# Kernel optimization log

Measured on AMD Instinct MI355X. Metric: run time of the kernel, lower is better.

Reference implementation:

```python
import jax, jax.numpy as jnp
import numpy as np

SEM_DIM = 256
N_LEVELS = 21
HALF = jnp.float32((N_LEVELS - 1) / 2.0)  # 10.0
BETA = 0.1  # commitment cost


def setup_inputs() -> dict:
    key = jax.random.key(0)
    k1, k2 = jax.random.split(key)
    z = jax.random.normal(k1, (8, 292, 2048), dtype=jnp.float32)
    # nn.init.uniform_(codebook.weight, -1/dim, 1/dim)
    codebook = jax.random.uniform(k2, (8192, SEM_DIM), dtype=jnp.float32,
                                  minval=-1.0 / SEM_DIM, maxval=1.0 / SEM_DIM)
    return {"z": z, "codebook": codebook}


def reference(z, codebook):
    # Split latent: semantic (VQ) / acoustic (FSQ)
    z_sem = z[:, :SEM_DIM, :]   # (B, 256, T)
    z_ac = z[:, SEM_DIM:, :]    # (B, 36, T)
    B, D, T = z_sem.shape

    # ---- VectorQuantizer (eval path) ----
    z_flat = jnp.transpose(z_sem, (0, 2, 1)).reshape(B * T, D)  # (BT, D)
    # ||z||^2 - 2 z.c^T + ||c||^2
    dists = (jnp.sum(z_flat * z_flat, axis=1, keepdims=True)
             - 2.0 * jnp.einsum('nd,kd->nk', z_flat, codebook)
             + jnp.sum(codebook * codebook, axis=1)[None, :])  # (BT, K)
    indices = jnp.argmin(dists, axis=1)  # (BT,)
    z_q = codebook[indices].reshape(B, T, D).transpose(0, 2, 1)  # (B, D, T)

    codebook_loss = jnp.mean((z_q - jax.lax.stop_gradient(z_sem)) ** 2)
    commitment_loss = BETA * jnp.mean((jax.lax.stop_gradient(z_q) - z_sem) ** 2)
    vq_loss = codebook_loss + commitment_loss

    # straight-through
    z_sem_q = z_sem + jax.lax.stop_gradient(z_q - z_sem)

    # ---- FSQ quantize (eval path) ----
    z_b = jnp.tanh(z_ac) * HALF
    z_ac_q = z_b + jax.lax.stop_gradient(jnp.round(z_b) - z_b)  # round STE
    ac_codes = jnp.clip(jnp.round(z_ac_q + HALF).astype(jnp.int32), 0, N_LEVELS - 1)

    z_out = jnp.concatenate([z_sem_q, z_ac_q], axis=1)  # (B, 292, T)
    return z_out, indices.reshape(B, T), ac_codes, vq_loss, z_ac_q
```

## Files before the change

kernel.cpp:

```cpp
#include <hip/hip_runtime.h>
#include <cfloat>
#include <math.h>

#define BQ 8
#define T 2048
#define D 256
#define DAC 36
#define CH 292
#define K 8192
#define NROWS (BQ*T)
#define TAU 1e-3f
#define FSPLIT 4
#define RSPLIT 16
#define CAPROWS 8192

#define OFF_IDX   (BQ*CH*T)
#define OFF_CODES (OFF_IDX + NROWS)
#define OFF_LOSS  (OFF_CODES + BQ*DAC*T)
#define OFF_ACQ   (OFF_LOSS + 1)

#define WN_C2    0
#define WN_Z2    32768
#define WN_CNT   98304
#define WN_LIST  98560
#define WN_LOSS  164096
#define WN_WIDX  168192
#define WN_PMX   262144
#define WN_PR    262144
#define WN_AZ    2359296
#define WN_ZG    2359296
#define WN_BC    10747904
#define WN_NEED  14942208

#define WS_C2    0
#define WS_Z2    32768
#define WS_PART  131072
#define WS_IDX   655360
#define WS_LOSS  720896
#define MT 32
#define KT 128
#define DC 32
#define NSPLIT 4

typedef float f32x4 __attribute__((ext_vector_type(4)));
typedef __bf16 bf16x8 __attribute__((ext_vector_type(8)));
typedef __attribute__((address_space(1))) const unsigned int gu32;
typedef __attribute__((address_space(3))) unsigned int lu32;

__device__ inline void gl_lds16(const void* gp, void* lp) {
    __builtin_amdgcn_global_load_lds((gu32*)gp, (lu32*)lp, 16, 0, 0);
}

__device__ inline unsigned short f2bf(float x) {
    unsigned u = __float_as_uint(x);
    return (unsigned short)((u + 0x7fffu + ((u >> 16) & 1u)) >> 16);
}

__device__ inline void merge3(float& m1, float& m2, int& mi, float o1, float o2, int oi) {
    if (o1 < m1 || (o1 == m1 && oi < mi)) { m2 = fminf(m1, o2); m1 = o1; mi = oi; }
    else                                  { m2 = fminf(m2, o1); }
}

template <typename F>
__device__ float np_pairwise256_sq(F ld) {
    float S[2];
    #pragma unroll
    for (int h = 0; h < 2; h++) {
        int base = h * 128;
        float v[16];
        #pragma unroll
        for (int l = 0; l < 16; l++) {
            float q[8];
            #pragma unroll
            for (int j = 0; j < 8; j++) { float x = ld(base + j * 16 + l); q[j] = x * x; }
            v[l] = ((q[0] + q[1]) + (q[2] + q[3])) + ((q[4] + q[5]) + (q[6] + q[7]));
        }
        float t1[8], t2[4], t3[2];
        #pragma unroll
        for (int l = 0; l < 8; l++) t1[l] = v[l] + v[l + 8];
        #pragma unroll
        for (int l = 0; l < 4; l++) t2[l] = t1[l] + t1[l + 4];
        t3[0] = t2[0] + t2[2]; t3[1] = t2[1] + t2[3];
        S[h] = t3[0] + t3[1];
    }
    return S[0] + S[1];
}

__global__ void k_c2pw(const float* __restrict__ cb, float* __restrict__ c2) {
    int k = blockIdx.x * 256 + threadIdx.x;
    const float* row = cb + (size_t)k * D;
    c2[k] = np_pairwise256_sq([&](int d) { return row[d]; });
}

__global__ void k_z2pw(const float* __restrict__ z, float* __restrict__ z2) {
    int n = blockIdx.x * 256 + threadIdx.x;
    int b = n >> 11, t = n & 2047;
    const float* base = z + (size_t)b * CH * T + t;
    z2[n] = np_pairwise256_sq([&](int d) { return base[(size_t)d * T]; });
}

__global__ __launch_bounds__(256) void k_prep(const float* __restrict__ z,
        const float* __restrict__ cb, unsigned short* __restrict__ Az,
        unsigned short* __restrict__ Bc, float* __restrict__ c2,
        float* __restrict__ z2, int* __restrict__ cnt, float* __restrict__ out) {
    __shared__ float zt[32][260];
    const int tid = threadIdx.x;
    if ((int)blockIdx.x < (K / 4)) {
        const int w = tid >> 6, l = tid & 63;
        const int k = blockIdx.x * 4 + w;
        float4 v = *(const float4*)(cb + (size_t)k * D + l * 4);
        *(float4*)&zt[w][l * 4] = v;
        float fa[4] = {v.x, v.y, v.z, v.w};
        unsigned short hh[4];
        #pragma unroll
        for (int e = 0; e < 4; e++) hh[e] = f2bf(fa[e]);
        *(uint2*)(Bc + (size_t)k * 256 + l * 4) = *(uint2*)hh;
        __syncthreads();
        if (tid < 4) {
            int kk = blockIdx.x * 4 + tid;
            c2[kk] = np_pairwise256_sq([&](int d) { return zt[tid][d]; });
        }
        if (blockIdx.x == 0 && tid == 0) *cnt = 0;
    } else if ((int)blockIdx.x < (K / 4) + 512) {
        const int bb = blockIdx.x - (K / 4);
        const int b = bb >> 6, t0 = (bb & 63) * 32;
        for (int i = tid; i < 2048; i += 256) {
            int d = i >> 3, tq = (i & 7) * 4;
            float4 v = *(const float4*)(z + (size_t)(b * CH + d) * T + t0 + tq);
            zt[tq + 0][d] = v.x; zt[tq + 1][d] = v.y;
            zt[tq + 2][d] = v.z; zt[tq + 3][d] = v.w;
        }
        __syncthreads();
        const int t = tid >> 3, c8 = tid & 7;
        unsigned short* rowp = Az + (size_t)(b * 2048 + t0 + t) * 256;
        #pragma unroll
        for (int li = 0; li < 4; li++) {
            int u = c8 + 8 * li;
            int dbase = u * 8;
            float f[8];
            *(float4*)&f[0] = *(float4*)&zt[t][dbase];
            *(float4*)&f[4] = *(float4*)&zt[t][dbase + 4];
            unsigned short h[8];
            #pragma unroll
            for (int e = 0; e < 8; e++) h[e] = f2bf(f[e]);
            *(uint4*)(rowp + u * 8) = *(uint4*)h;
        }
        if (tid < 32)
            z2[b * 2048 + t0 + tid] = np_pairwise256_sq([&](int d) { return zt[tid][d]; });
    } else {
        const int ab = blockIdx.x - ((K / 4) + 512);
        int i = (ab * 256 + tid) * 4;
        int b = i / (DAC * T);
        int r = i % (DAC * T);
        int d = r / T, t = r % T;
        size_t zoff = ((size_t)(b * CH + 256 + d)) * T + t;
        float4 v = *(const float4*)(z + zoff);
        float r0, r1, r2, r3;
        {
            float t0 = (float)tanh((double)v.x); r0 = rintf(t0 * 10.0f);
            float t1 = (float)tanh((double)v.y); r1 = rintf(t1 * 10.0f);
            float t2 = (float)tanh((double)v.z); r2 = rintf(t2 * 10.0f);
            float t3 = (float)tanh((double)v.w); r3 = rintf(t3 * 10.0f);
        }
        *(float4*)(out + zoff) = make_float4(r0, r1, r2, r3);
        size_t co = OFF_CODES + (size_t)(b * DAC + d) * T + t;
        *(float4*)(out + co) = make_float4(r0 + 10.0f, r1 + 10.0f, r2 + 10.0f, r3 + 10.0f);
        size_t ao = OFF_ACQ + (size_t)(b * DAC + d) * T + t;
        out[ao + 0] = r0; out[ao + 1] = r1; out[ao + 2] = r2; out[ao + 3] = r3;
    }
}

__global__ __launch_bounds__(256, 2) void k_fast(
        const unsigned short* __restrict__ Az, const unsigned short* __restrict__ Bc,
        const float* __restrict__ c2g, float4* __restrict__ pmx) {
    __shared__ __align__(16) unsigned char smem8[65536];
    __shared__ float c2s[2048];

    const int tid = threadIdx.x;
    const int w = tid >> 6, lane = tid & 63;
    const int quad = lane >> 4, c = lane & 15;

    const int sp = blockIdx.x >> 7;
    const int nt = blockIdx.x & 127;
    const int n0 = nt * 128;
    const int kbase = sp * 2048;

    const char* Azb = (const char*)Az;
    const char* Bcb = (const char*)Bc;

    #pragma unroll
    for (int i = 0; i < 8; i++) c2s[tid + i * 256] = c2g[kbase + tid + i * 256];

    const int hi2 = lane >> 5;
    const char* sq[8];
    #pragma unroll
    for (int q = 0; q < 8; q++) {
        const int seg = w * 8 + q;
        const int code = seg * 2 + hi2;
        sq[q] = Bcb + (size_t)(kbase + code) * 512 + (((lane & 31) ^ (code & 7)) << 4);
    }
    auto stage = [&](int t, int buf) {
        unsigned char* base = smem8 + buf * 32768;
        #pragma unroll
        for (int q = 0; q < 8; q++)
            gl_lds16(sq[q] + (size_t)t * 32768, base + (w * 8 + q) * 1024);
    };

    int voff[8];
    #pragma unroll
    for (int ks = 0; ks < 8; ks++)
        voff[ks] = c * 512 + (((((ks << 2) | quad) ^ (c & 7))) << 4);

    bf16x8 af[2][8];
    #pragma unroll
    for (int i = 0; i < 2; i++)
        #pragma unroll
        for (int ks = 0; ks < 8; ks++)
            af[i][ks] = *(const bf16x8*)(Azb +
                (size_t)(n0 + w * 32 + i * 16 + c) * 512 + ks * 64 + quad * 16);

    float bm1[8], bm2[8]; int bid[8];
    #pragma unroll
    for (int sl = 0; sl < 8; sl++) { bm1[sl] = FLT_MAX; bm2[sl] = FLT_MAX; bid[sl] = 0x7fffffff; }

    f32x4 accA[2][4], accB[2][4];

    #define MFMA_TILE(BUFC, ACC) do {                                         \
        _Pragma("unroll")                                                     \
        for (int i = 0; i < 2; i++)                                           \
            _Pragma("unroll")                                                 \
            for (int j = 0; j < 4; j++) ACC[i][j] = (f32x4)0.0f;              \
        _Pragma("unroll")                                                     \
        for (int j = 0; j < 4; j++) {                                         \
            bf16x8 bf[8];                                                     \
            _Pragma("unroll")                                                 \
            for (int ks = 0; ks < 8; ks++)                                    \
                bf[ks] = *(const bf16x8*)(smem8 + voff[ks] +                  \
                                          ((BUFC) * 32768 + j * 8192));       \
            _Pragma("unroll")                                                 \
            for (int ks = 0; ks < 8; ks++) {                 \
                ACC[0][j] = __builtin_amdgcn_mfma_f32_16x16x32_bf16(af[0][ks], bf[ks], ACC[0][j], 0, 0, 0); \
                ACC[1][j] = __builtin_amdgcn_mfma_f32_16x16x32_bf16(af[1][ks], bf[ks], ACC[1][j], 0, 0, 0); \
            }                                                                 \
        }                                                                     \
    } while (0)

    auto epilogue = [&](int t, f32x4 (&acc)[2][4]) {
        const int k0 = kbase + t * 64;
        #pragma unroll
        for (int j = 0; j < 4; j++) {
            const int kk = k0 + j * 16 + c;
            const float c2v = c2s[t * 64 + j * 16 + c];
            #pragma unroll
            for (int i = 0; i < 2; i++)
                #pragma unroll
                for (int r = 0; r < 4; r++) {
                    float sc = fmaf(-2.0f, acc[i][j][r], c2v);
                    int sl = i * 4 + r;
                    if (sc < bm1[sl]) { bm2[sl] = bm1[sl]; bm1[sl] = sc; bid[sl] = kk; }
                    else if (sc < bm2[sl]) bm2[sl] = sc;
                }
        }
    };

    stage(0, 0);
    __syncthreads();
    stage(1, 1);
    MFMA_TILE(0, accA);

    #define FITER(T, BUF, CUR, PRV) do {                                  \
        asm volatile("s_waitcnt vmcnt(0)" ::: "memory");                  \
        __builtin_amdgcn_s_barrier();                                     \
        __builtin_amdgcn_sched_barrier(0);                                \
        if ((T) < 31) stage((T) + 1, (BUF) ^ 1);                          \
        MFMA_TILE(BUF, CUR);                                              \
        epilogue((T) - 1, PRV);                                           \
    } while (0)

    for (int tt = 1; tt < 31; tt += 2) {
        FITER(tt,     1, accB, accA);
        FITER(tt + 1, 0, accA, accB);
    }
    FITER(31, 1, accB, accA);
    epilogue(31, accB);
    #undef FITER
    #undef MFMA_TILE

    #pragma unroll
    for (int mask = 1; mask <= 8; mask <<= 1)
        #pragma unroll
        for (int sl = 0; sl < 8; sl++) {
            float o1 = __shfl_xor(bm1[sl], mask, 64);
            float o2 = __shfl_xor(bm2[sl], mask, 64);
            int   oi = __shfl_xor(bid[sl], mask, 64);
            merge3(bm1[sl], bm2[sl], bid[sl], o1, o2, oi);
        }
    if (c == 0) {
        #pragma unroll
        for (int i = 0; i < 2; i++)
            #pragma unroll
            for (int r = 0; r < 4; r++) {
                int row = w * 32 + i * 16 + quad * 4 + r, sl = i * 4 + r;
                pmx[(size_t)sp * NROWS + n0 + row] =
                    make_float4(bm1[sl], bm2[sl], __int_as_float(bid[sl]), 0.f);
            }
    }
}

__global__ void k_reduce2(const float4* __restrict__ pmx, int* __restrict__ widx,
                          int* __restrict__ cnt, int* __restrict__ list,
                          float* __restrict__ out) {
    int n = blockIdx.x * 256 + threadIdx.x;
    float a1 = FLT_MAX, a2 = FLT_MAX; int ai = 0x7fffffff;
    #pragma unroll
    for (int s = 0; s < FSPLIT; s++) {
        float4 p = pmx[(size_t)s * NROWS + n];
        merge3(a1, a2, ai, p.x, p.y, __float_as_int(p.z));
    }
    widx[n] = ai;
    out[OFF_IDX + n] = (float)ai;
    if (a2 - a1 < TAU) { int pos = atomicAdd(cnt, 1); list[pos] = n; }
}

__global__ __launch_bounds__(256) void k_gz(const float* __restrict__ z,
        const int* __restrict__ cnt, const int* __restrict__ list,
        float* __restrict__ zg) {
    const int base = blockIdx.x * MT;
    const int cntv = min(*cnt, CAPROWS);
    if (base >= cntv) return;
    const int nr = min(MT, cntv - base);
    __shared__ int ls[MT];
    const int tid = threadIdx.x;
    if (tid < MT) ls[tid] = list[base + ((tid < nr) ? tid : (nr - 1))];
    __syncthreads();
    for (int it = 0; it < MT; it++) {
        int n = ls[it];
        zg[(size_t)(base + it) * D + tid] =
            z[((size_t)((n >> 11) * CH + tid)) * T + (n & 2047)];
    }
}

__global__ __launch_bounds__(256, 2) void k_rescuex(
        const float* __restrict__ z, const float* __restrict__ cb,
        const float* __restrict__ c2, const float* __restrict__ z2,
        const int* __restrict__ cnt, const int* __restrict__ list,
        const float* __restrict__ zg, float2* __restrict__ pr) {
    __shared__ float zs[D][MT + 4];
    __shared__ float cs[2][DC][KT + 4];
    __shared__ float c2s[K / RSPLIT];
    __shared__ int   ls[MT];
    __shared__ float z2sh[MT];
    const int tid = threadIdx.x;
    const int tx = tid & 31, ty = tid >> 5;
    const int grp = blockIdx.x >> 4, sp = blockIdx.x & 15;
    const int cntv = *cnt;
    const int base = grp * MT;
    if (base >= cntv) return;
    const int nr = min(MT, cntv - base);
    const int kbase = sp * (K / RSPLIT);
    const int kl = tid & 127, half = tid >> 7;

    if (tid < MT) {
        int pos = base + ((tid < nr) ? tid : (nr - 1));
        int n = list[pos];
        ls[tid] = n;
        z2sh[tid] = z2[n];
    }
    #pragma unroll
    for (int i = 0; i < (K / RSPLIT) / 256; i++)
        c2s[tid + i * 256] = c2[kbase + tid + i * 256];

    float4 rv0, rv1, rv2, rv3;
    auto ldchunk = [&](int ch) {
        const int k0 = kbase + (ch >> 3) * KT, dcc = (ch & 7) * DC;
        const float4* src = (const float4*)(cb + (size_t)(k0 + kl) * D + dcc + half * 16);
        rv0 = src[0]; rv1 = src[1]; rv2 = src[2]; rv3 = src[3];
    };
    auto wrchunk = [&](int b) {
        const int dl = half * 16;
        cs[b][dl + 0][kl] = rv0.x; cs[b][dl + 1][kl] = rv0.y;
        cs[b][dl + 2][kl] = rv0.z; cs[b][dl + 3][kl] = rv0.w;
        cs[b][dl + 4][kl] = rv1.x; cs[b][dl + 5][kl] = rv1.y;
        cs[b][dl + 6][kl] = rv1.z; cs[b][dl + 7][kl] = rv1.w;
        cs[b][dl + 8][kl] = rv2.x; cs[b][dl + 9][kl] = rv2.y;
        cs[b][dl + 10][kl] = rv2.z; cs[b][dl + 11][kl] = rv2.w;
        cs[b][dl + 12][kl] = rv3.x; cs[b][dl + 13][kl] = rv3.y;
        cs[b][dl + 14][kl] = rv3.z; cs[b][dl + 15][kl] = rv3.w;
    };

    if (base + MT <= CAPROWS) {
        ldchunk(0);
        for (int i = tid; i < MT * 64; i += 256) {
            int r = i >> 6, dq = (i & 63) << 2;
            float4 v = *(const float4*)(zg + (size_t)(base + r) * D + dq);
            zs[dq + 0][r] = v.x; zs[dq + 1][r] = v.y;
            zs[dq + 2][r] = v.z; zs[dq + 3][r] = v.w;
        }
    } else {
        __syncthreads();
        for (int i = tid; i < D * MT; i += 256) {
            int d = i >> 5, r = i & 31;
            int n = ls[r];
            zs[d][r] = z[((size_t)((n >> 11) * CH + d)) * T + (n & 2047)];
        }
        ldchunk(0);
    }
    __syncthreads();
    wrchunk(0);
    ldchunk(1);
    asm volatile("s_waitcnt lgkmcnt(0)" ::: "memory");
    __builtin_amdgcn_s_barrier();
    __builtin_amdgcn_sched_barrier(0);

    float z2r[4];
    #pragma unroll
    for (int i = 0; i < 4; i++) z2r[i] = z2sh[ty * 4 + i];

    float m1[4]; int bi[4];
    #pragma unroll
    for (int i = 0; i < 4; i++) { m1[i] = FLT_MAX; bi[i] = 0x7fffffff; }
    float acc[4][4] = {};

    const int NCH = (K / RSPLIT) / KT * (D / DC);
    for (int ch = 0; ch < NCH; ch++) {
        const int b = ch & 1;
        const int dcc = (ch & 7) * DC;
        #pragma unroll 8
        for (int d = 0; d < DC; d++) {
            const float4 zf = *(const float4*)&zs[dcc + d][ty * 4];
            const float4 cf = *(const float4*)&cs[b][d][tx * 4];
            const float za[4] = {zf.x, zf.y, zf.z, zf.w};
            const float ca[4] = {cf.x, cf.y, cf.z, cf.w};
            #pragma unroll
            for (int i = 0; i < 4; i++)
                #pragma unroll
                for (int j = 0; j < 4; j++)
                    acc[i][j] = fmaf(za[i], ca[j], acc[i][j]);
        }
        if ((ch & 7) == 7) {
            const int koff = (ch >> 3) * KT;
            #pragma unroll
            for (int j = 0; j < 4; j++) {
                int kk = kbase + koff + tx * 4 + j;
                float c2v = c2s[koff + tx * 4 + j];
                #pragma unroll
                for (int i = 0; i < 4; i++) {
                    float tpre = z2r[i] - 2.0f * acc[i][j];
                    float s = tpre + c2v;
                    if (s < m1[i]) { m1[i] = s; bi[i] = kk; }
                }
            }
            #pragma unroll
            for (int i = 0; i < 4; i++)
                #pragma unroll
                for (int j = 0; j < 4; j++) acc[i][j] = 0.0f;
        }
        if (ch < NCH - 1) {
            __syncthreads();
            wrchunk(b ^ 1);
            if (ch < NCH - 2) ldchunk(ch + 2);
            asm volatile("s_waitcnt lgkmcnt(0)" ::: "memory");
            __builtin_amdgcn_s_barrier();
            __builtin_amdgcn_sched_barrier(0);
        }
    }
    __syncthreads();
    float* rm1 = (float*)zs;
    int*   rix = (int*)(rm1 + MT * 32);
    #pragma unroll
    for (int i = 0; i < 4; i++) {
        int slot = (ty * 4 + i) * 32 + tx;
        rm1[slot] = m1[i]; rix[slot] = bi[i];
    }
    __syncthreads();
    if (tid < MT) {
        float a1 = FLT_MAX; int ai = 0x7fffffff;
        for (int t = 0; t < 32; t++) {
            float b1 = rm1[tid * 32 + t]; int bidx = rix[tid * 32 + t];
            if (b1 < a1 || (b1 == a1 && bidx < ai)) { a1 = b1; ai = bidx; }
        }
        if (tid < nr)
            pr[(size_t)sp * NROWS + base + tid] = make_float2(a1, __int_as_float(ai));
    }
}

__global__ void k_unpack(const float2* __restrict__ pr, const int* __restrict__ cnt,
                         const int* __restrict__ list, int* __restrict__ widx,
                         float* __restrict__ out) {
    int pos = blockIdx.x * 256 + threadIdx.x;
    if (pos >= *cnt) return;
    float a1 = FLT_MAX; int ai = 0x7fffffff;
    #pragma unroll
    for (int s = 0; s < RSPLIT; s++) {
        float2 p = pr[(size_t)s * NROWS + pos];
        float v = p.x; int ix = __float_as_int(p.y);
        if (v < a1 || (v == a1 && ix < ai)) { a1 = v; ai = ix; }
    }
    int n = list[pos];
    widx[n] = ai;
    out[OFF_IDX + n] = (float)ai;
}

__global__ __launch_bounds__(256) void k_exact(
        const float* __restrict__ z, const float* __restrict__ cb,
        const float* __restrict__ c2, const float* __restrict__ z2,
        float2* __restrict__ part) {
    __shared__ float zs[D][MT];
    __shared__ float cs[DC][KT + 4];
    const int tid = threadIdx.x;
    const int tx = tid & 31, ty = tid >> 5;
    const int n0 = blockIdx.x * MT;
    const int bb = n0 >> 11, t0 = n0 & 2047;
    const int kbase = blockIdx.y * (K / NSPLIT);
    for (int i = tid; i < D * (MT / 4); i += 256) {
        int d = i >> 3, tg = i & 7;
        float4 v = *(const float4*)(z + ((size_t)(bb * CH + d)) * T + t0 + tg * 4);
        *(float4*)&zs[d][tg * 4] = v;
    }
    float z2r[4];
    #pragma unroll
    for (int i = 0; i < 4; i++) z2r[i] = z2[n0 + ty * 4 + i];
    float m1[4]; int bi[4];
    #pragma unroll
    for (int i = 0; i < 4; i++) { m1[i] = FLT_MAX; bi[i] = 0x7fffffff; }
    for (int ktt = 0; ktt < K / NSPLIT; ktt += KT) {
        const int k0 = kbase + ktt;
        float acc[4][4] = {};
        for (int dc = 0; dc < D; dc += DC) {
            __syncthreads();
            {
                int kl = tid & 127, half = tid >> 7;
                const float4* src = (const float4*)(cb + (size_t)(k0 + kl) * D + dc + half * 16);
                #pragma unroll
                for (int j = 0; j < 4; j++) {
                    float4 v = src[j];
                    int dl = half * 16 + j * 4;
                    cs[dl + 0][kl] = v.x; cs[dl + 1][kl] = v.y;
                    cs[dl + 2][kl] = v.z; cs[dl + 3][kl] = v.w;
                }
            }
            __syncthreads();
            #pragma unroll 8
            for (int d = 0; d < DC; d++) {
                const float4 zf = *(const float4*)&zs[dc + d][ty * 4];
                const float4 cf = *(const float4*)&cs[d][tx * 4];
                const float za[4] = {zf.x, zf.y, zf.z, zf.w};
                const float ca[4] = {cf.x, cf.y, cf.z, cf.w};
                #pragma unroll
                for (int i = 0; i < 4; i++)
                    #pragma unroll
                    for (int j = 0; j < 4; j++)
                        acc[i][j] = fmaf(za[i], ca[j], acc[i][j]);
            }
        }
        #pragma unroll
        for (int j = 0; j < 4; j++) {
            int kk = k0 + tx * 4 + j;
            float c2v = c2[kk];
            #pragma unroll
            for (int i = 0; i < 4; i++) {
                float tpre = z2r[i] - 2.0f * acc[i][j];
                float s = tpre + c2v;
                if (s < m1[i]) { m1[i] = s; bi[i] = kk; }
            }
        }
    }
    __syncthreads();
    float* rm1 = (float*)zs;
    int*   rix = (int*)(rm1 + MT * 32);
    #pragma unroll
    for (int i = 0; i < 4; i++) {
        int slot = (ty * 4 + i) * 32 + tx;
        rm1[slot] = m1[i]; rix[slot] = bi[i];
    }
    __syncthreads();
    if (tid < MT) {
        float a1 = FLT_MAX; int ai = 0x7fffffff;
        for (int t = 0; t < 32; t++) {
            float b1 = rm1[tid * 32 + t]; int bidx = rix[tid * 32 + t];
            if (b1 < a1 || (b1 == a1 && bidx < ai)) { a1 = b1; ai = bidx; }
        }
        part[(size_t)(n0 + tid) * NSPLIT + blockIdx.y] = make_float2(a1, __int_as_float(ai));
    }
}

__global__ void k_reduce(const float2* __restrict__ part, int* __restrict__ widx,
                         float* __restrict__ out) {
    int n = blockIdx.x * 256 + threadIdx.x;
    float a1 = FLT_MAX; int ai = 0x7fffffff;
    #pragma unroll
    for (int s = 0; s < NSPLIT; s++) {
        float2 p = part[(size_t)n * NSPLIT + s];
        float b1 = p.x; int bidx = __float_as_int(p.y);
        if (b1 < a1 || (b1 == a1 && bidx < ai)) { a1 = b1; ai = bidx; }
    }
    widx[n] = ai;
    out[OFF_IDX + n] = (float)ai;
}

__global__ __launch_bounds__(256) void k_episem(
        const float* __restrict__ z, const float* __restrict__ cb,
        const int* __restrict__ widx, float* __restrict__ out, double* __restrict__ lossp) {
    __shared__ int qidx[32];
    __shared__ float qs[32][260];
    __shared__ double wsum[4];
    const int tid = threadIdx.x;
    const int bb = blockIdx.x >> 6;
    const int t0 = (blockIdx.x & 63) * 32;
    if (tid < 32) qidx[tid] = widx[bb * T + t0 + tid];
    __syncthreads();
    for (int i = tid; i < 32 * 64; i += 256) {
        int tl = i >> 6, lanee = i & 63;
        float4 v = *(const float4*)(cb + (size_t)qidx[tl] * D + lanee * 4);
        *(float4*)&qs[tl][lanee * 4] = v;
    }
    __syncthreads();
    double ls = 0.0;
    for (int it = 0; it < 32; it++) {
        int d = it * 8 + (tid >> 5);
        int tl = tid & 31;
        size_t ga = ((size_t)(bb * CH + d)) * T + t0 + tl;
        float q = qs[tl][d];
        float e = q - z[ga];
        out[ga] = q;
        ls += (double)e * (double)e;
    }
    #pragma unroll
    for (int off = 32; off; off >>= 1) ls += __shfl_down(ls, off, 64);
    if ((tid & 63) == 0) wsum[tid >> 6] = ls;
    __syncthreads();
    if (tid == 0) lossp[blockIdx.x] = wsum[0] + wsum[1] + wsum[2] + wsum[3];
}

__global__ void k_loss(const double* __restrict__ lossp, float* __restrict__ out) {
    __shared__ double sm[256];
    int tid = threadIdx.x;
    sm[tid] = lossp[tid] + lossp[tid + 256];
    __syncthreads();
    for (int off = 128; off; off >>= 1) {
        if (tid < off) sm[tid] += sm[tid + off];
        __syncthreads();
    }
    if (tid == 0) out[OFF_LOSS] = (float)(1.1 * sm[0] / (double)(BQ * D * T));
}

__global__ void k_epiac(const float* __restrict__ z, const double* __restrict__ lossp,
                        float* __restrict__ out) {
    __shared__ double sm[256];
    int i = (blockIdx.x * 256 + threadIdx.x) * 4;
    int b = i / (DAC * T);
    int r = i % (DAC * T);
    int d = r / T, t = r % T;
    size_t zoff = ((size_t)(b * CH + 256 + d)) * T + t;
    float4 v = *(const float4*)(z + zoff);
    float r0, r1, r2, r3;
    {
        float t0 = (float)tanh((double)v.x); r0 = rintf(t0 * 10.0f);
        float t1 = (float)tanh((double)v.y); r1 = rintf(t1 * 10.0f);
        float t2 = (float)tanh((double)v.z); r2 = rintf(t2 * 10.0f);
        float t3 = (float)tanh((double)v.w); r3 = rintf(t3 * 10.0f);
    }
    *(float4*)(out + zoff) = make_float4(r0, r1, r2, r3);
    size_t co = OFF_CODES + (size_t)(b * DAC + d) * T + t;
    *(float4*)(out + co) = make_float4(r0 + 10.0f, r1 + 10.0f, r2 + 10.0f, r3 + 10.0f);
    size_t ao = OFF_ACQ + (size_t)(b * DAC + d) * T + t;
    out[ao + 0] = r0; out[ao + 1] = r1; out[ao + 2] = r2; out[ao + 3] = r3;
    if (blockIdx.x == 0) {
        int tid = threadIdx.x;
        sm[tid] = lossp[tid] + lossp[tid + 256];
        __syncthreads();
        for (int off = 128; off; off >>= 1) {
            if (tid < off) sm[tid] += sm[tid + off];
            __syncthreads();
        }
        if (tid == 0) out[OFF_LOSS] = (float)(1.1 * sm[0] / (double)(BQ * D * T));
    }
}

extern "C" void kernel_launch(void* const* d_in, const int* in_sizes, int n_in,
                              void* d_out, int out_size, void* d_ws, size_t ws_size,
                              hipStream_t stream) {
    const float* z  = (const float*)d_in[0];
    const float* cb = (const float*)d_in[1];
    float* out = (float*)d_out;
    char* ws = (char*)d_ws;

    if (ws_size >= (size_t)WN_NEED) {
        float*  c2    = (float*)(ws + WN_C2);
        float*  z2    = (float*)(ws + WN_Z2);
        int*    cnt   = (int*)(ws + WN_CNT);
        int*    list  = (int*)(ws + WN_LIST);
        double* lossp = (double*)(ws + WN_LOSS);
        int*    widx  = (int*)(ws + WN_WIDX);
        float4* pmx   = (float4*)(ws + WN_PMX);
        unsigned short* Az = (unsigned short*)(ws + WN_AZ);
        unsigned short* Bc = (unsigned short*)(ws + WN_BC);
        float*  zg    = (float*)(ws + WN_ZG);
        float2* pr    = (float2*)(ws + WN_PR);

        hipLaunchKernelGGL(k_prep,    dim3(K / 4 + 512 + BQ * DAC * T / 1024), dim3(256), 0, stream,
                           z, cb, Az, Bc, c2, z2, cnt, out);
        hipLaunchKernelGGL(k_fast,    dim3(128 * FSPLIT), dim3(256), 0, stream, Az, Bc, c2, pmx);
        hipLaunchKernelGGL(k_reduce2, dim3(NROWS / 256),  dim3(256), 0, stream, pmx, widx, cnt, list, out);
        hipLaunchKernelGGL(k_gz,      dim3(CAPROWS / MT), dim3(256), 0, stream, z, cnt, list, zg);
        hipLaunchKernelGGL(k_rescuex, dim3((NROWS / MT) * RSPLIT), dim3(256), 0, stream,
                           z, cb, c2, z2, cnt, list, zg, pr);
        hipLaunchKernelGGL(k_unpack,  dim3(NROWS / 256),  dim3(256), 0, stream, pr, cnt, list, widx, out);
        hipLaunchKernelGGL(k_episem,  dim3(BQ * (T / 32)), dim3(256), 0, stream, z, cb, widx, out, lossp);
        hipLaunchKernelGGL(k_loss,    dim3(1),            dim3(256), 0, stream, lossp, out);
    } else {
        float*  c2    = (float*)(ws + WS_C2);
        float*  z2    = (float*)(ws + WS_Z2);
        float2* part  = (float2*)(ws + WS_PART);
        int*    widx  = (int*)(ws + WS_IDX);
        double* lossp = (double*)(ws + WS_LOSS);
        hipLaunchKernelGGL(k_c2pw,   dim3(K / 256),            dim3(256), 0, stream, cb, c2);
        hipLaunchKernelGGL(k_z2pw,   dim3(NROWS / 256),        dim3(256), 0, stream, z, z2);
        hipLaunchKernelGGL(k_exact,  dim3(NROWS / MT, NSPLIT), dim3(256), 0, stream, z, cb, c2, z2, part);
        hipLaunchKernelGGL(k_reduce, dim3(NROWS / 256),        dim3(256), 0, stream, part, widx, out);
        hipLaunchKernelGGL(k_episem, dim3(BQ * (T / 32)),      dim3(256), 0, stream, z, cb, widx, out, lossp);
        hipLaunchKernelGGL(k_epiac,  dim3(BQ * DAC * T / 1024), dim3(256), 0, stream, z, lossp, out);
    }
}
```

Measured before the change: 292.8 us.

## Fuse gather into reduce, fold unpack into episem, add MFMA priority and med3

The k_gz gather is folded into k_reduce2: each block records its ambiguous rows in shared memory and copies their z rows into zg directly. The k_unpack kernel is removed. Rescued rows are marked in widx with a negated list position, and k_episem merges the RSPLIT partial results for those rows itself. This removes two kernel launches and their global round trips. The MFMA loop also raises wave priority with s_setprio, and the running second-best update becomes a branch-free fmed3. A k_episemf copy keeps the fallback path unchanged.

Result: faster. 269.0 us (-8.1%).

```diff
diff --git a/kernel.cpp b/kernel.cpp
--- a/kernel.cpp
+++ b/kernel.cpp
@@ -230,6 +230,7 @@
         for (int i = 0; i < 2; i++)                                           \
             _Pragma("unroll")                                                 \
             for (int j = 0; j < 4; j++) ACC[i][j] = (f32x4)0.0f;              \
+        __builtin_amdgcn_s_setprio(1);                                        \
         _Pragma("unroll")                                                     \
         for (int j = 0; j < 4; j++) {                                         \
             bf16x8 bf[8];                                                     \
@@ -243,6 +244,7 @@
                 ACC[1][j] = __builtin_amdgcn_mfma_f32_16x16x32_bf16(af[1][ks], bf[ks], ACC[1][j], 0, 0, 0); \
             }                                                                 \
         }                                                                     \
+        __builtin_amdgcn_s_setprio(0);                                        \
     } while (0)
 
     auto epilogue = [&](int t, f32x4 (&acc)[2][4]) {
@@ -257,8 +259,8 @@
                 for (int r = 0; r < 4; r++) {
                     float sc = fmaf(-2.0f, acc[i][j][r], c2v);
                     int sl = i * 4 + r;
-                    if (sc < bm1[sl]) { bm2[sl] = bm1[sl]; bm1[sl] = sc; bid[sl] = kk; }
-                    else if (sc < bm2[sl]) bm2[sl] = sc;
+                    bm2[sl] = __builtin_amdgcn_fmed3f(bm1[sl], sc, bm2[sl]);
+                    if (sc < bm1[sl]) { bm1[sl] = sc; bid[sl] = kk; }
                 }
         }
     };
@@ -307,36 +309,42 @@
     }
 }
 
-__global__ void k_reduce2(const float4* __restrict__ pmx, int* __restrict__ widx,
+__global__ __launch_bounds__(256) void k_reduce2(const float4* __restrict__ pmx,
+                          int* __restrict__ widx,
                           int* __restrict__ cnt, int* __restrict__ list,
-                          float* __restrict__ out) {
-    int n = blockIdx.x * 256 + threadIdx.x;
+                          float* __restrict__ out, const float* __restrict__ z,
+                          float* __restrict__ zg) {
+    __shared__ int lrow[256], lpos[256];
+    __shared__ int lcnt;
+    const int tid = threadIdx.x;
+    if (tid == 0) lcnt = 0;
+    __syncthreads();
+    int n = blockIdx.x * 256 + tid;
     float a1 = FLT_MAX, a2 = FLT_MAX; int ai = 0x7fffffff;
     #pragma unroll
     for (int s = 0; s < FSPLIT; s++) {
         float4 p = pmx[(size_t)s * NROWS + n];
         merge3(a1, a2, ai, p.x, p.y, __float_as_int(p.z));
     }
-    widx[n] = ai;
-    out[OFF_IDX + n] = (float)ai;
-    if (a2 - a1 < TAU) { int pos = atomicAdd(cnt, 1); list[pos] = n; }
-}
-
-__global__ __launch_bounds__(256) void k_gz(const float* __restrict__ z,
-        const int* __restrict__ cnt, const int* __restrict__ list,
-        float* __restrict__ zg) {
-    const int base = blockIdx.x * MT;
-    const int cntv = min(*cnt, CAPROWS);
-    if (base >= cntv) return;
-    const int nr = min(MT, cntv - base);
-    __shared__ int ls[MT];
-    const int tid = threadIdx.x;
-    if (tid < MT) ls[tid] = list[base + ((tid < nr) ? tid : (nr - 1))];
-    __syncthreads();
-    for (int it = 0; it < MT; it++) {
-        int n = ls[it];
-        zg[(size_t)(base + it) * D + tid] =
-            z[((size_t)((n >> 11) * CH + tid)) * T + (n & 2047)];
+    if (a2 - a1 < TAU) {
+        int pos = atomicAdd(cnt, 1);
+        list[pos] = n;
+        widx[n] = ~pos;
+        int l = atomicAdd(&lcnt, 1);
+        lrow[l] = n; lpos[l] = pos;
+    } else {
+        widx[n] = ai;
+        out[OFF_IDX + n] = (float)ai;
+    }
+    __syncthreads();
+    const int lc = lcnt;
+    for (int it = 0; it < lc; it++) {
+        int pos = lpos[it];
+        if (pos < CAPROWS) {
+            int rn = lrow[it];
+            zg[(size_t)pos * D + tid] =
+                z[((size_t)((rn >> 11) * CH + tid)) * T + (rn & 2047)];
+        }
     }
 }
 
@@ -482,23 +490,6 @@
         if (tid < nr)
             pr[(size_t)sp * NROWS + base + tid] = make_float2(a1, __int_as_float(ai));
     }
-}
-
-__global__ void k_unpack(const float2* __restrict__ pr, const int* __restrict__ cnt,
-                         const int* __restrict__ list, int* __restrict__ widx,
-                         float* __restrict__ out) {
-    int pos = blockIdx.x * 256 + threadIdx.x;
-    if (pos >= *cnt) return;
-    float a1 = FLT_MAX; int ai = 0x7fffffff;
-    #pragma unroll
-    for (int s = 0; s < RSPLIT; s++) {
-        float2 p = pr[(size_t)s * NROWS + pos];
-        float v = p.x; int ix = __float_as_int(p.y);
-        if (v < a1 || (v == a1 && ix < ai)) { a1 = v; ai = ix; }
-    }
-    int n = list[pos];
-    widx[n] = ai;
-    out[OFF_IDX + n] = (float)ai;
 }
 
 __global__ __launch_bounds__(256) void k_exact(
@@ -600,14 +591,31 @@
 
 __global__ __launch_bounds__(256) void k_episem(
         const float* __restrict__ z, const float* __restrict__ cb,
-        const int* __restrict__ widx, float* __restrict__ out, double* __restrict__ lossp) {
+        const int* __restrict__ widx, const float2* __restrict__ pr,
+        float* __restrict__ out, double* __restrict__ lossp) {
     __shared__ int qidx[32];
     __shared__ float qs[32][260];
     __shared__ double wsum[4];
     const int tid = threadIdx.x;
     const int bb = blockIdx.x >> 6;
     const int t0 = (blockIdx.x & 63) * 32;
-    if (tid < 32) qidx[tid] = widx[bb * T + t0 + tid];
+    if (tid < 32) {
+        int n = bb * T + t0 + tid;
+        int wv = widx[n];
+        if (wv < 0) {
+            int pos = ~wv;
+            float a1 = FLT_MAX; int ai = 0x7fffffff;
+            #pragma unroll
+            for (int s = 0; s < RSPLIT; s++) {
+                float2 p = pr[(size_t)s * NROWS + pos];
+                float v = p.x; int ix = __float_as_int(p.y);
+                if (v < a1 || (v == a1 && ix < ai)) { a1 = v; ai = ix; }
+            }
+            wv = ai;
+            out[OFF_IDX + n] = (float)ai;
+        }
+        qidx[tid] = wv;
+    }
     __syncthreads();
     for (int i = tid; i < 32 * 64; i += 256) {
         int tl = i >> 6, lanee = i & 63;
@@ -642,6 +650,40 @@
         __syncthreads();
     }
     if (tid == 0) out[OFF_LOSS] = (float)(1.1 * sm[0] / (double)(BQ * D * T));
+}
+
+__global__ __launch_bounds__(256) void k_episemf(
+        const float* __restrict__ z, const float* __restrict__ cb,
+        const int* __restrict__ widx, float* __restrict__ out, double* __restrict__ lossp) {
+    __shared__ int qidx[32];
+    __shared__ float qs[32][260];
+    __shared__ double wsum[4];
+    const int tid = threadIdx.x;
+    const int bb = blockIdx.x >> 6;
+    const int t0 = (blockIdx.x & 63) * 32;
+    if (tid < 32) qidx[tid] = widx[bb * T + t0 + tid];
+    __syncthreads();
+    for (int i = tid; i < 32 * 64; i += 256) {
+        int tl = i >> 6, lanee = i & 63;
+        float4 v = *(const float4*)(cb + (size_t)qidx[tl] * D + lanee * 4);
+        *(float4*)&qs[tl][lanee * 4] = v;
+    }
+    __syncthreads();
+    double ls = 0.0;
+    for (int it = 0; it < 32; it++) {
+        int d = it * 8 + (tid >> 5);
+        int tl = tid & 31;
+        size_t ga = ((size_t)(bb * CH + d)) * T + t0 + tl;
+        float q = qs[tl][d];
+        float e = q - z[ga];
+        out[ga] = q;
+        ls += (double)e * (double)e;
+    }
+    #pragma unroll
+    for (int off = 32; off; off >>= 1) ls += __shfl_down(ls, off, 64);
+    if ((tid & 63) == 0) wsum[tid >> 6] = ls;
+    __syncthreads();
+    if (tid == 0) lossp[blockIdx.x] = wsum[0] + wsum[1] + wsum[2] + wsum[3];
 }
 
 __global__ void k_epiac(const float* __restrict__ z, const double* __restrict__ lossp,
@@ -701,12 +743,12 @@
         hipLaunchKernelGGL(k_prep,    dim3(K / 4 + 512 + BQ * DAC * T / 1024), dim3(256), 0, stream,
                            z, cb, Az, Bc, c2, z2, cnt, out);
         hipLaunchKernelGGL(k_fast,    dim3(128 * FSPLIT), dim3(256), 0, stream, Az, Bc, c2, pmx);
-        hipLaunchKernelGGL(k_reduce2, dim3(NROWS / 256),  dim3(256), 0, stream, pmx, widx, cnt, list, out);
-        hipLaunchKernelGGL(k_gz,      dim3(CAPROWS / MT), dim3(256), 0, stream, z, cnt, list, zg);
+        hipLaunchKernelGGL(k_reduce2, dim3(NROWS / 256),  dim3(256), 0, stream,
+                           pmx, widx, cnt, list, out, z, zg);
         hipLaunchKernelGGL(k_rescuex, dim3((NROWS / MT) * RSPLIT), dim3(256), 0, stream,
                            z, cb, c2, z2, cnt, list, zg, pr);
-        hipLaunchKernelGGL(k_unpack,  dim3(NROWS / 256),  dim3(256), 0, stream, pr, cnt, list, widx, out);
-        hipLaunchKernelGGL(k_episem,  dim3(BQ * (T / 32)), dim3(256), 0, stream, z, cb, widx, out, lossp);
+        hipLaunchKernelGGL(k_episem,  dim3(BQ * (T / 32)), dim3(256), 0, stream,
+                           z, cb, widx, pr, out, lossp);
         hipLaunchKernelGGL(k_loss,    dim3(1),            dim3(256), 0, stream, lossp, out);
     } else {
         float*  c2    = (float*)(ws + WS_C2);
@@ -718,7 +760,7 @@
         hipLaunchKernelGGL(k_z2pw,   dim3(NROWS / 256),        dim3(256), 0, stream, z, z2);
         hipLaunchKernelGGL(k_exact,  dim3(NROWS / MT, NSPLIT), dim3(256), 0, stream, z, cb, c2, z2, part);
         hipLaunchKernelGGL(k_reduce, dim3(NROWS / 256),        dim3(256), 0, stream, part, widx, out);
-        hipLaunchKernelGGL(k_episem, dim3(BQ * (T / 32)),      dim3(256), 0, stream, z, cb, widx, out, lossp);
+        hipLaunchKernelGGL(k_episemf, dim3(BQ * (T / 32)),     dim3(256), 0, stream, z, cb, widx, out, lossp);
         hipLaunchKernelGGL(k_epiac,  dim3(BQ * DAC * T / 1024), dim3(256), 0, stream, z, lossp, out);
     }
 }
```
